# Performance work log

Measured on AMD Instinct MI355X. Metric: run time of the kernel, lower is better.

The kernel has to match this reference:

```python
import jax, jax.numpy as jnp
import numpy as np

B, T, IN_DIM = 128, 4096, 13
UNITS, MOTOR = 64, 6
LAYERS = [35, 23, 6]   # AutoNCP(64, 6): inter / command / motor neurons
_SPLITS = [35, 58]     # cumulative layer boundaries inside the 64-unit state


def setup_inputs() -> dict:
    keys = iter(jax.random.split(jax.random.key(0), 64))
    def rn(shape, s=0.1):
        return jax.random.normal(next(keys), shape, dtype=jnp.float32) * s
    inp = {"x": jax.random.normal(next(keys), (B, T, IN_DIM), dtype=jnp.float32)}
    # mixed-memory LSTM cell (ncps: input_map has bias, recurrent_map does not)
    inp["lstm_wi"] = rn((4 * UNITS, IN_DIM))
    inp["lstm_wh"] = rn((4 * UNITS, UNITS))
    inp["lstm_b"] = rn((4 * UNITS,))
    # wired CfC layers: ff1/ff2/time_a/time_b acting on concat([input, h])
    in_dims = [IN_DIM] + LAYERS[:-1]
    for i, (d, h) in enumerate(zip(in_dims, LAYERS)):
        for nm in ("w1", "w2", "wa", "wb"):
            inp[f"cfc{i}_{nm}"] = rn((h, d + h))
        for nm in ("b1", "b2", "ba", "bb"):
            inp[f"cfc{i}_{nm}"] = rn((h,))
    inp["gyro_w1"] = rn((32, MOTOR)); inp["gyro_b1"] = rn((32,))
    inp["gyro_w2"] = rn((3, 32));     inp["gyro_b2"] = rn((3,))
    inp["acc_w1"] = rn((32, MOTOR));  inp["acc_b1"] = rn((32,))
    inp["acc_w2"] = rn((3, 32));      inp["acc_b2"] = rn((3,))
    inp["unc_w1"] = rn((16, MOTOR));  inp["unc_b1"] = rn((16,))
    inp["unc_w2"] = rn((6, 16));      inp["unc_b2"] = rn((6,))
    return inp


def _cfc_step(inp, h, p):
    """ncps CfCCell, mode='default', no backbone, ts = 1.0."""
    W1, b1, W2, b2, Wa, ba, Wb, bb = p
    z = jnp.concatenate([inp, h], axis=-1)            # (B, in+hid)
    ff1 = jnp.tanh(z @ W1.T + b1)
    ff2 = jnp.tanh(z @ W2.T + b2)
    t = jax.nn.sigmoid((z @ Wa.T + ba) + (z @ Wb.T + bb))  # t_a*ts + t_b, ts==1
    return ff1 * (1.0 - t) + t * ff2


def reference(x, lstm_wi, lstm_wh, lstm_b,
              cfc0_w1, cfc0_b1, cfc0_w2, cfc0_b2, cfc0_wa, cfc0_ba, cfc0_wb, cfc0_bb,
              cfc1_w1, cfc1_b1, cfc1_w2, cfc1_b2, cfc1_wa, cfc1_ba, cfc1_wb, cfc1_bb,
              cfc2_w1, cfc2_b1, cfc2_w2, cfc2_b2, cfc2_wa, cfc2_ba, cfc2_wb, cfc2_bb,
              gyro_w1, gyro_b1, gyro_w2, gyro_b2,
              acc_w1, acc_b1, acc_w2, acc_b2,
              unc_w1, unc_b1, unc_w2, unc_b2):
    layer_params = (
        (cfc0_w1, cfc0_b1, cfc0_w2, cfc0_b2, cfc0_wa, cfc0_ba, cfc0_wb, cfc0_bb),
        (cfc1_w1, cfc1_b1, cfc1_w2, cfc1_b2, cfc1_wa, cfc1_ba, cfc1_wb, cfc1_bb),
        (cfc2_w1, cfc2_b1, cfc2_w2, cfc2_b2, cfc2_wa, cfc2_ba, cfc2_wb, cfc2_bb),
    )

    def step(carry, xt):  # xt: (B, 13)
        h, c = carry
        # mixed-memory LSTM over the full 64-unit state (forget gate +1.0)
        zg = xt @ lstm_wi.T + lstm_b + h @ lstm_wh.T
        ia, ig, fg, og = jnp.split(zg, 4, axis=-1)
        c_new = c * jax.nn.sigmoid(fg + 1.0) + jnp.tanh(ia) * jax.nn.sigmoid(ig)
        h_lstm = jnp.tanh(c_new) * jax.nn.sigmoid(og)
        # wired CfC: inter -> command -> motor, each fed previous layer's output
        hs = jnp.split(h_lstm, _SPLITS, axis=-1)
        inp = xt
        new_hs = []
        for hi, p in zip(hs, layer_params):
            inp = _cfc_step(inp, hi, p)
            new_hs.append(inp)
        return (jnp.concatenate(new_hs, axis=-1), c_new), inp  # motor out (B,6)

    Bsz = x.shape[0]
    h0 = jnp.zeros((Bsz, UNITS), x.dtype)
    c0 = jnp.zeros((Bsz, UNITS), x.dtype)
    _, outs = jax.lax.scan(step, (h0, c0), jnp.swapaxes(x, 0, 1))
    cfc_out = jnp.swapaxes(outs, 0, 1)  # (B, T, 6)

    gyro = jnp.tanh(cfc_out @ gyro_w1.T + gyro_b1) @ gyro_w2.T + gyro_b2
    acc = jnp.tanh(cfc_out @ acc_w1.T + acc_b1) @ acc_w2.T + acc_b2
    pred = jnp.concatenate([gyro, acc], axis=-1)                      # (B, T, 6)
    unc = jax.nn.softplus(
        jax.nn.relu(cfc_out @ unc_w1.T + unc_b1) @ unc_w2.T + unc_b2)  # (B, T, 6)
    return pred, unc
```

## Files before the change

kernel.cpp:

```cpp
#include <hip/hip_runtime.h>
#include <math.h>

#define BATCH 128
#define TSTEPS 4096
#define INDIM 13
#define XT 64


__device__ __forceinline__ float fsig(float x) {
    return __builtin_amdgcn_rcpf(1.f + __expf(-x));
}
__device__ __forceinline__ float ftanh(float x) {
    float s = fsig(x + x);
    return s + s - 1.f;
}
__device__ __forceinline__ float fsoftplus(float x) {
    return (x > 15.f) ? x : __logf(1.f + __expf(x));
}

__device__ __forceinline__ float qxor1(float v) {
    return __int_as_float(__builtin_amdgcn_update_dpp(
        0, __float_as_int(v), 0xB1, 0xF, 0xF, true));
}
__device__ __forceinline__ float qxor2(float v) {
    return __int_as_float(__builtin_amdgcn_update_dpp(
        0, __float_as_int(v), 0x4E, 0xF, 0xF, true));
}
#define BFLY4(a) { a += qxor1(a); a += qxor2(a); }

#define FMA4(acc, W, q, zv) { acc += zv.x * W##_##q##_0; acc += zv.y * W##_##q##_1; \
                              acc += zv.z * W##_##q##_2; acc += zv.w * W##_##q##_3; }

__global__ __launch_bounds__(256, 1)
void rnn_kernel(const float* __restrict__ x,
                const float* __restrict__ lstm_wi, const float* __restrict__ lstm_wh,
                const float* __restrict__ lstm_b,
                const float* __restrict__ c0w1, const float* __restrict__ c0w2,
                const float* __restrict__ c0wa, const float* __restrict__ c0wb,
                const float* __restrict__ c0b1, const float* __restrict__ c0b2,
                const float* __restrict__ c0ba, const float* __restrict__ c0bb,
                const float* __restrict__ c1w1, const float* __restrict__ c1w2,
                const float* __restrict__ c1wa, const float* __restrict__ c1wb,
                const float* __restrict__ c1b1, const float* __restrict__ c1b2,
                const float* __restrict__ c1ba, const float* __restrict__ c1bb,
                const float* __restrict__ c2w1, const float* __restrict__ c2w2,
                const float* __restrict__ c2wa, const float* __restrict__ c2wb,
                const float* __restrict__ c2b1, const float* __restrict__ c2b2,
                const float* __restrict__ c2ba, const float* __restrict__ c2bb,
                float* __restrict__ out)
{
    const int bb = blockIdx.x;
    const int t  = threadIdx.x;
    const int k  = t & 3;
    const int u  = t >> 2;

    __shared__ __align__(16) float smem[2688];
    float* zL  = smem;
    float* z0  = smem + 96;
    float* z1  = smem + 160;
    float* z2  = smem + 224;
    float* xt0 = smem + 256;
    float* xt1 = smem + 1088;
    float* ot0 = smem + 1920;
    float* ot1 = smem + 2304;

    const long xbase = (long)bb * TSTEPS * INDIM;
    const long obase = (long)bb * TSTEPS * 6;

    auto lwf = [&](int A, int c) -> float {
        int r = A * 64 + u;
        return (c < 13) ? lstm_wi[r * 13 + c]
             : (c < 77) ? lstm_wh[r * 64 + (c - 13)] : 0.f;
    };
#define DEF_WL(A,q) \
    float wl##A##_##q##_0 = lwf(A, 24*k + 4*q + 0); \
    float wl##A##_##q##_1 = lwf(A, 24*k + 4*q + 1); \
    float wl##A##_##q##_2 = lwf(A, 24*k + 4*q + 2); \
    float wl##A##_##q##_3 = lwf(A, 24*k + 4*q + 3);
    DEF_WL(0,0) DEF_WL(0,1) DEF_WL(0,2) DEF_WL(0,3) DEF_WL(0,4) DEF_WL(0,5)
    DEF_WL(1,0) DEF_WL(1,1) DEF_WL(1,2) DEF_WL(1,3) DEF_WL(1,4) DEF_WL(1,5)
    DEF_WL(2,0) DEF_WL(2,1) DEF_WL(2,2) DEF_WL(2,3) DEF_WL(2,4) DEF_WL(2,5)
    DEF_WL(3,0) DEF_WL(3,1) DEF_WL(3,2) DEF_WL(3,3) DEF_WL(3,4) DEF_WL(3,5)
#undef DEF_WL
    const float bL0 = lstm_b[u];
    const float bL1 = lstm_b[64 + u];
    const float bL2 = lstm_b[128 + u];
    const float bL3 = lstm_b[192 + u];

    const int grp  = (u < 35) ? 0 : (u < 58) ? 1 : 2;
    const int row  = (grp == 0) ? u : (grp == 1) ? (u - 35) : (u - 58);
    const int rl   = (grp == 0) ? 48 : (grp == 1) ? 58 : 29;
    const int clen = (grp == 0) ? 12 : (grp == 1) ? 16 : 8;
    const int cb   = clen * k;
    const float *W0p, *W1p, *W2p, *W3p;
    float bC0, bC1, bC2, bC3;
    if (grp == 0) {
        W0p = c0w1 + row * 48; W1p = c0w2 + row * 48;
        W2p = c0wa + row * 48; W3p = c0wb + row * 48;
        bC0 = c0b1[row]; bC1 = c0b2[row]; bC2 = c0ba[row]; bC3 = c0bb[row];
    } else if (grp == 1) {
        W0p = c1w1 + row * 58; W1p = c1w2 + row * 58;
        W2p = c1wa + row * 58; W3p = c1wb + row * 58;
        bC0 = c1b1[row]; bC1 = c1b2[row]; bC2 = c1ba[row]; bC3 = c1bb[row];
    } else {
        W0p = c2w1 + row * 29; W1p = c2w2 + row * 29;
        W2p = c2wa + row * 29; W3p = c2wb + row * 29;
        bC0 = c2b1[row]; bC1 = c2b2[row]; bC2 = c2ba[row]; bC3 = c2bb[row];
    }
    auto cwf = [&](const float* W, int c) -> float {
        int cc = cb + c;
        return (c < clen && cc < rl) ? W[cc] : 0.f;
    };
#define DEF_WC(A,q) \
    float wc##A##_##q##_0 = cwf(W##A##p, 4*q + 0); \
    float wc##A##_##q##_1 = cwf(W##A##p, 4*q + 1); \
    float wc##A##_##q##_2 = cwf(W##A##p, 4*q + 2); \
    float wc##A##_##q##_3 = cwf(W##A##p, 4*q + 3);
    DEF_WC(0,0) DEF_WC(0,1) DEF_WC(0,2) DEF_WC(0,3)
    DEF_WC(1,0) DEF_WC(1,1) DEF_WC(1,2) DEF_WC(1,3)
    DEF_WC(2,0) DEF_WC(2,1) DEF_WC(2,2) DEF_WC(2,3)
    DEF_WC(3,0) DEF_WC(3,1) DEF_WC(3,2) DEF_WC(3,3)
#undef DEF_WC

    float creg = 0.f;

    smem[t] = 0.f;
    if (t < 208) {
        float4 xi = *(const float4*)(x + xbase + 4 * t);
        *(float4*)&xt0[4 * t] = xi;
    }
    if (t < 13) { float x0 = x[xbase + t]; zL[t] = x0; z0[t] = x0; }
    __syncthreads();

    #pragma unroll 1
    for (int ts = 0; ts < TSTEPS; ++ts) {
        const int par = (ts >> 6) & 1;
        const int lts = ts & 63;

        {
            const float4* zc = (const float4*)(zL + 24 * k);
            float4 q0 = zc[0], q1 = zc[1], q2 = zc[2],
                   q3 = zc[3], q4 = zc[4], q5 = zc[5];
            float a0 = 0.f, a1 = 0.f, a2 = 0.f, a3 = 0.f;
            FMA4(a0, wl0, 0, q0) FMA4(a0, wl0, 1, q1) FMA4(a0, wl0, 2, q2)
            FMA4(a0, wl0, 3, q3) FMA4(a0, wl0, 4, q4) FMA4(a0, wl0, 5, q5)
            FMA4(a1, wl1, 0, q0) FMA4(a1, wl1, 1, q1) FMA4(a1, wl1, 2, q2)
            FMA4(a1, wl1, 3, q3) FMA4(a1, wl1, 4, q4) FMA4(a1, wl1, 5, q5)
            FMA4(a2, wl2, 0, q0) FMA4(a2, wl2, 1, q1) FMA4(a2, wl2, 2, q2)
            FMA4(a2, wl2, 3, q3) FMA4(a2, wl2, 4, q4) FMA4(a2, wl2, 5, q5)
            FMA4(a3, wl3, 0, q0) FMA4(a3, wl3, 1, q1) FMA4(a3, wl3, 2, q2)
            FMA4(a3, wl3, 3, q3) FMA4(a3, wl3, 4, q4) FMA4(a3, wl3, 5, q5)
            BFLY4(a0) BFLY4(a1) BFLY4(a2) BFLY4(a3)
            a0 += bL0; a1 += bL1; a2 += bL2; a3 += bL3;
            float cn = creg * fsig(a2 + 1.f) + ftanh(a0) * fsig(a1);
            creg = cn;
            float hl = ftanh(cn) * fsig(a3);
            if (k == 0) {
                if (u < 35)      z0[13 + u] = hl;
                else if (u < 58) z1[u]      = hl;
                else             z2[u - 35] = hl;
            }
        }
        __syncthreads();

        if (grp == 0) {
            const float4* zc = (const float4*)(z0 + 12 * k);
            float4 v0 = zc[0], v1 = zc[1], v2 = zc[2];
            float a0 = 0.f, a1 = 0.f, a2 = 0.f, a3 = 0.f;
            FMA4(a0, wc0, 0, v0) FMA4(a0, wc0, 1, v1) FMA4(a0, wc0, 2, v2)
            FMA4(a1, wc1, 0, v0) FMA4(a1, wc1, 1, v1) FMA4(a1, wc1, 2, v2)
            FMA4(a2, wc2, 0, v0) FMA4(a2, wc2, 1, v1) FMA4(a2, wc2, 2, v2)
            FMA4(a3, wc3, 0, v0) FMA4(a3, wc3, 1, v1) FMA4(a3, wc3, 2, v2)
            BFLY4(a0) BFLY4(a1) BFLY4(a2) BFLY4(a3)
            a0 += bC0; a1 += bC1; a2 += bC2; a3 += bC3;
            float tg = fsig(a2 + a3);
            float f1 = ftanh(a0), f2 = ftanh(a1);
            float o = f1 + tg * (f2 - f1);
            if (k == 0) { z1[row] = o; zL[13 + row] = o; }
        } else {
            if (lts == 62 && (ts + 2) < TSTEPS) {
                int i = (t - 140) * 2;
                float* dst = par ? xt0 : xt1;
                const float* src = x + xbase + (long)(ts + 2) * 13;
                if (i < 208)     *(float4*)&dst[4*i]     = *(const float4*)(src + 4*i);
                if (i + 1 < 208) *(float4*)&dst[4*(i+1)] = *(const float4*)(src + 4*(i+1));
            }
            if (lts == 0 && ts > 0) {
                int i = t - 140;
                if (i < 96) {
                    const float* src = par ? ot0 : ot1;
                    float4 v = *(const float4*)&src[4 * i];
                    *(float4*)(out + obase + (long)(ts - XT) * 6 + 4 * i) = v;
                }
            }
        }
        __syncthreads();

        if (grp == 1) {
            const float4* zc = (const float4*)(z1 + 16 * k);
            float4 v0 = zc[0], v1 = zc[1], v2 = zc[2], v3 = zc[3];
            float a0 = 0.f, a1 = 0.f, a2 = 0.f, a3 = 0.f;
            FMA4(a0, wc0, 0, v0) FMA4(a0, wc0, 1, v1) FMA4(a0, wc0, 2, v2) FMA4(a0, wc0, 3, v3)
            FMA4(a1, wc1, 0, v0) FMA4(a1, wc1, 1, v1) FMA4(a1, wc1, 2, v2) FMA4(a1, wc1, 3, v3)
            FMA4(a2, wc2, 0, v0) FMA4(a2, wc2, 1, v1) FMA4(a2, wc2, 2, v2) FMA4(a2, wc2, 3, v3)
            FMA4(a3, wc3, 0, v0) FMA4(a3, wc3, 1, v1) FMA4(a3, wc3, 2, v2) FMA4(a3, wc3, 3, v3)
            BFLY4(a0) BFLY4(a1) BFLY4(a2) BFLY4(a3)
            a0 += bC0; a1 += bC1; a2 += bC2; a3 += bC3;
            float tg = fsig(a2 + a3);
            float f1 = ftanh(a0), f2 = ftanh(a1);
            float o = f1 + tg * (f2 - f1);
            if (k == 0) { z2[row] = o; zL[48 + row] = o; }
        }
        __syncthreads();

        if (grp == 2) {
            const float4* zc = (const float4*)(z2 + 8 * k);
            float4 v0 = zc[0], v1 = zc[1];
            float a0 = 0.f, a1 = 0.f, a2 = 0.f, a3 = 0.f;
            FMA4(a0, wc0, 0, v0) FMA4(a0, wc0, 1, v1)
            FMA4(a1, wc1, 0, v0) FMA4(a1, wc1, 1, v1)
            FMA4(a2, wc2, 0, v0) FMA4(a2, wc2, 1, v1)
            FMA4(a3, wc3, 0, v0) FMA4(a3, wc3, 1, v1)
            BFLY4(a0) BFLY4(a1) BFLY4(a2) BFLY4(a3)
            a0 += bC0; a1 += bC1; a2 += bC2; a3 += bC3;
            float tg = fsig(a2 + a3);
            float f1 = ftanh(a0), f2 = ftanh(a1);
            float o = f1 + tg * (f2 - f1);
            if (k == 0) {
                zL[71 + row] = o;
                float* ob = par ? ot1 : ot0;
                ob[lts * 6 + row] = o;
            }
        } else if (t < 13 && (ts + 1) < TSTEPS) {
            const float* xb = (((ts + 1) >> 6) & 1) ? xt1 : xt0;
            float xn = xb[((ts + 1) & 63) * 13 + t];
            zL[t] = xn; z0[t] = xn;
        }
        __syncthreads();
    }

    if (t < 96) {
        float4 v = *(const float4*)&ot1[4 * t];
        *(float4*)(out + obase + (long)(TSTEPS - XT) * 6 + 4 * t) = v;
    }
}

#define S_GW1 0
#define S_GB1 192
#define S_GW2 224
#define S_GB2 320
#define S_AW1 323
#define S_AB1 515
#define S_AW2 547
#define S_AB2 643
#define S_UW1 646
#define S_UB1 742
#define S_UW2 758
#define S_UB2 854
#define S_TOT 860

__global__ __launch_bounds__(256)
void head_kernel(const float* __restrict__ gw1, const float* __restrict__ gb1,
                 const float* __restrict__ gw2, const float* __restrict__ gb2,
                 const float* __restrict__ aw1, const float* __restrict__ ab1,
                 const float* __restrict__ aw2, const float* __restrict__ ab2,
                 const float* __restrict__ uw1, const float* __restrict__ ub1,
                 const float* __restrict__ uw2, const float* __restrict__ ub2,
                 float* __restrict__ out)
{
    __shared__ float s[S_TOT];
    const int t = threadIdx.x;
    if (t < 192) { s[S_GW1 + t] = gw1[t]; s[S_AW1 + t] = aw1[t]; }
    if (t < 96)  { s[S_GW2 + t] = gw2[t]; s[S_AW2 + t] = aw2[t];
                   s[S_UW1 + t] = uw1[t]; s[S_UW2 + t] = uw2[t]; }
    if (t < 32)  { s[S_GB1 + t] = gb1[t]; s[S_AB1 + t] = ab1[t]; }
    if (t < 16)  { s[S_UB1 + t] = ub1[t]; }
    if (t < 3)   { s[S_GB2 + t] = gb2[t]; s[S_AB2 + t] = ab2[t]; }
    if (t < 6)   { s[S_UB2 + t] = ub2[t]; }
    __syncthreads();

    const long p = (long)blockIdx.x * 256 + t;
    const long base = p * 6;
    float m0 = out[base+0], m1 = out[base+1], m2 = out[base+2];
    float m3 = out[base+3], m4 = out[base+4], m5 = out[base+5];

    float gy0 = s[S_GB2+0], gy1 = s[S_GB2+1], gy2 = s[S_GB2+2];
    float ac0 = s[S_AB2+0], ac1 = s[S_AB2+1], ac2 = s[S_AB2+2];
    #pragma unroll
    for (int i = 0; i < 32; ++i) {
        float hg = s[S_GB1+i] + s[S_GW1+i*6+0]*m0 + s[S_GW1+i*6+1]*m1
                 + s[S_GW1+i*6+2]*m2 + s[S_GW1+i*6+3]*m3
                 + s[S_GW1+i*6+4]*m4 + s[S_GW1+i*6+5]*m5;
        hg = ftanh(hg);
        gy0 += s[S_GW2+i]*hg; gy1 += s[S_GW2+32+i]*hg; gy2 += s[S_GW2+64+i]*hg;
        float ha = s[S_AB1+i] + s[S_AW1+i*6+0]*m0 + s[S_AW1+i*6+1]*m1
                 + s[S_AW1+i*6+2]*m2 + s[S_AW1+i*6+3]*m3
                 + s[S_AW1+i*6+4]*m4 + s[S_AW1+i*6+5]*m5;
        ha = ftanh(ha);
        ac0 += s[S_AW2+i]*ha; ac1 += s[S_AW2+32+i]*ha; ac2 += s[S_AW2+64+i]*ha;
    }
    float u0 = s[S_UB2+0], u1 = s[S_UB2+1], u2 = s[S_UB2+2];
    float u3 = s[S_UB2+3], u4 = s[S_UB2+4], u5 = s[S_UB2+5];
    #pragma unroll
    for (int i = 0; i < 16; ++i) {
        float hu = s[S_UB1+i] + s[S_UW1+i*6+0]*m0 + s[S_UW1+i*6+1]*m1
                 + s[S_UW1+i*6+2]*m2 + s[S_UW1+i*6+3]*m3
                 + s[S_UW1+i*6+4]*m4 + s[S_UW1+i*6+5]*m5;
        hu = fmaxf(hu, 0.f);
        u0 += s[S_UW2+i]*hu;      u1 += s[S_UW2+16+i]*hu; u2 += s[S_UW2+32+i]*hu;
        u3 += s[S_UW2+48+i]*hu;   u4 += s[S_UW2+64+i]*hu; u5 += s[S_UW2+80+i]*hu;
    }
    out[base+0] = gy0; out[base+1] = gy1; out[base+2] = gy2;
    out[base+3] = ac0; out[base+4] = ac1; out[base+5] = ac2;
    const long uoff = (long)BATCH * TSTEPS * 6;
    out[uoff+base+0] = fsoftplus(u0); out[uoff+base+1] = fsoftplus(u1);
    out[uoff+base+2] = fsoftplus(u2); out[uoff+base+3] = fsoftplus(u3);
    out[uoff+base+4] = fsoftplus(u4); out[uoff+base+5] = fsoftplus(u5);
}

extern "C" void kernel_launch(void* const* d_in, const int* in_sizes, int n_in,
                              void* d_out, int out_size, void* d_ws, size_t ws_size,
                              hipStream_t stream) {
    const float* x       = (const float*)d_in[0];
    const float* lstm_wi = (const float*)d_in[1];
    const float* lstm_wh = (const float*)d_in[2];
    const float* lstm_b  = (const float*)d_in[3];
    const float* c0w1 = (const float*)d_in[4];
    const float* c0w2 = (const float*)d_in[5];
    const float* c0wa = (const float*)d_in[6];
    const float* c0wb = (const float*)d_in[7];
    const float* c0b1 = (const float*)d_in[8];
    const float* c0b2 = (const float*)d_in[9];
    const float* c0ba = (const float*)d_in[10];
    const float* c0bb = (const float*)d_in[11];
    const float* c1w1 = (const float*)d_in[12];
    const float* c1w2 = (const float*)d_in[13];
    const float* c1wa = (const float*)d_in[14];
    const float* c1wb = (const float*)d_in[15];
    const float* c1b1 = (const float*)d_in[16];
    const float* c1b2 = (const float*)d_in[17];
    const float* c1ba = (const float*)d_in[18];
    const float* c1bb = (const float*)d_in[19];
    const float* c2w1 = (const float*)d_in[20];
    const float* c2w2 = (const float*)d_in[21];
    const float* c2wa = (const float*)d_in[22];
    const float* c2wb = (const float*)d_in[23];
    const float* c2b1 = (const float*)d_in[24];
    const float* c2b2 = (const float*)d_in[25];
    const float* c2ba = (const float*)d_in[26];
    const float* c2bb = (const float*)d_in[27];
    const float* gw1 = (const float*)d_in[28];
    const float* gb1 = (const float*)d_in[29];
    const float* gw2 = (const float*)d_in[30];
    const float* gb2 = (const float*)d_in[31];
    const float* aw1 = (const float*)d_in[32];
    const float* ab1 = (const float*)d_in[33];
    const float* aw2 = (const float*)d_in[34];
    const float* ab2 = (const float*)d_in[35];
    const float* uw1 = (const float*)d_in[36];
    const float* ub1 = (const float*)d_in[37];
    const float* uw2 = (const float*)d_in[38];
    const float* ub2 = (const float*)d_in[39];
    float* out = (float*)d_out;

    rnn_kernel<<<BATCH, 256, 0, stream>>>(x, lstm_wi, lstm_wh, lstm_b,
        c0w1, c0w2, c0wa, c0wb, c0b1, c0b2, c0ba, c0bb,
        c1w1, c1w2, c1wa, c1wb, c1b1, c1b2, c1ba, c1bb,
        c2w1, c2w2, c2wa, c2wb, c2b1, c2b2, c2ba, c2bb, out);

    head_kernel<<<(BATCH * TSTEPS) / 256, 256, 0, stream>>>(
        gw1, gb1, gw2, gb2, aw1, ab1, aw2, ab2, uw1, ub1, uw2, ub2, out);
}
```

Before: 5.327 ms.

## Process two batch sequences per block to share barriers and add ILP

Each block now runs the recurrence for two batch elements, interleaving their LSTM and CfC step computations, with shared-memory state, input tiles and output staging duplicated per sequence. The grid is halved to 64 blocks. The aim is to spread the fixed per-step barrier and latency cost over two independent dependency chains, giving the scheduler more independent work to overlap. The trade-off is roughly twice the arithmetic per step on the critical path and half as many blocks, which may lengthen each step if the latency is not fully hidden.

```diff
diff --git a/kernel.cpp b/kernel.cpp
--- a/kernel.cpp
+++ b/kernel.cpp
@@ -49,23 +49,16 @@
                 const float* __restrict__ c2ba, const float* __restrict__ c2bb,
                 float* __restrict__ out)
 {
-    const int bb = blockIdx.x;
     const int t  = threadIdx.x;
     const int k  = t & 3;
     const int u  = t >> 2;
 
-    __shared__ __align__(16) float smem[2688];
-    float* zL  = smem;
-    float* z0  = smem + 96;
-    float* z1  = smem + 160;
-    float* z2  = smem + 224;
-    float* xt0 = smem + 256;
-    float* xt1 = smem + 1088;
-    float* ot0 = smem + 1920;
-    float* ot1 = smem + 2304;
-
-    const long xbase = (long)bb * TSTEPS * INDIM;
-    const long obase = (long)bb * TSTEPS * 6;
+    __shared__ __align__(16) float smem[5376];
+
+    const long xbase[2] = {(long)(2*blockIdx.x)     * TSTEPS * INDIM,
+                           (long)(2*blockIdx.x + 1) * TSTEPS * INDIM};
+    const long obase[2] = {(long)(2*blockIdx.x)     * TSTEPS * 6,
+                           (long)(2*blockIdx.x + 1) * TSTEPS * 6};
 
     auto lwf = [&](int A, int c) -> float {
         int r = A * 64 + u;
@@ -122,14 +115,16 @@
     DEF_WC(3,0) DEF_WC(3,1) DEF_WC(3,2) DEF_WC(3,3)
 #undef DEF_WC
 
-    float creg = 0.f;
-
-    smem[t] = 0.f;
+    float creg[2] = {0.f, 0.f};
+
+    for (int i = t; i < 512; i += 256) smem[i] = 0.f;
     if (t < 208) {
-        float4 xi = *(const float4*)(x + xbase + 4 * t);
-        *(float4*)&xt0[4 * t] = xi;
-    }
-    if (t < 13) { float x0 = x[xbase + t]; zL[t] = x0; z0[t] = x0; }
+        *(float4*)&smem[512 + 4*t]        = *(const float4*)(x + xbase[0] + 4*t);
+        *(float4*)&smem[512 + 1664 + 4*t] = *(const float4*)(x + xbase[1] + 4*t);
+    }
+    if (t < 13)               { float v = x[xbase[0] + t]; smem[t] = v; smem[96 + t] = v; }
+    if (t >= 16 && t < 29)    { int i = t - 16;
+                                float v = x[xbase[1] + i]; smem[256 + i] = v; smem[256 + 96 + i] = v; }
     __syncthreads();
 
     #pragma unroll 1
@@ -138,110 +133,143 @@
         const int lts = ts & 63;
 
         {
-            const float4* zc = (const float4*)(zL + 24 * k);
-            float4 q0 = zc[0], q1 = zc[1], q2 = zc[2],
-                   q3 = zc[3], q4 = zc[4], q5 = zc[5];
-            float a0 = 0.f, a1 = 0.f, a2 = 0.f, a3 = 0.f;
-            FMA4(a0, wl0, 0, q0) FMA4(a0, wl0, 1, q1) FMA4(a0, wl0, 2, q2)
-            FMA4(a0, wl0, 3, q3) FMA4(a0, wl0, 4, q4) FMA4(a0, wl0, 5, q5)
-            FMA4(a1, wl1, 0, q0) FMA4(a1, wl1, 1, q1) FMA4(a1, wl1, 2, q2)
-            FMA4(a1, wl1, 3, q3) FMA4(a1, wl1, 4, q4) FMA4(a1, wl1, 5, q5)
-            FMA4(a2, wl2, 0, q0) FMA4(a2, wl2, 1, q1) FMA4(a2, wl2, 2, q2)
-            FMA4(a2, wl2, 3, q3) FMA4(a2, wl2, 4, q4) FMA4(a2, wl2, 5, q5)
-            FMA4(a3, wl3, 0, q0) FMA4(a3, wl3, 1, q1) FMA4(a3, wl3, 2, q2)
-            FMA4(a3, wl3, 3, q3) FMA4(a3, wl3, 4, q4) FMA4(a3, wl3, 5, q5)
-            BFLY4(a0) BFLY4(a1) BFLY4(a2) BFLY4(a3)
-            a0 += bL0; a1 += bL1; a2 += bL2; a3 += bL3;
-            float cn = creg * fsig(a2 + 1.f) + ftanh(a0) * fsig(a1);
-            creg = cn;
-            float hl = ftanh(cn) * fsig(a3);
-            if (k == 0) {
-                if (u < 35)      z0[13 + u] = hl;
-                else if (u < 58) z1[u]      = hl;
-                else             z2[u - 35] = hl;
+            float4 q[2][6];
+            #pragma unroll
+            for (int e = 0; e < 2; ++e) {
+                const float4* zc = (const float4*)(smem + e*256 + 24*k);
+                q[e][0]=zc[0]; q[e][1]=zc[1]; q[e][2]=zc[2];
+                q[e][3]=zc[3]; q[e][4]=zc[4]; q[e][5]=zc[5];
+            }
+            #pragma unroll
+            for (int e = 0; e < 2; ++e) {
+                float a0 = 0.f, a1 = 0.f, a2 = 0.f, a3 = 0.f;
+                FMA4(a0, wl0, 0, q[e][0]) FMA4(a0, wl0, 1, q[e][1]) FMA4(a0, wl0, 2, q[e][2])
+                FMA4(a0, wl0, 3, q[e][3]) FMA4(a0, wl0, 4, q[e][4]) FMA4(a0, wl0, 5, q[e][5])
+                FMA4(a1, wl1, 0, q[e][0]) FMA4(a1, wl1, 1, q[e][1]) FMA4(a1, wl1, 2, q[e][2])
+                FMA4(a1, wl1, 3, q[e][3]) FMA4(a1, wl1, 4, q[e][4]) FMA4(a1, wl1, 5, q[e][5])
+                FMA4(a2, wl2, 0, q[e][0]) FMA4(a2, wl2, 1, q[e][1]) FMA4(a2, wl2, 2, q[e][2])
+                FMA4(a2, wl2, 3, q[e][3]) FMA4(a2, wl2, 4, q[e][4]) FMA4(a2, wl2, 5, q[e][5])
+                FMA4(a3, wl3, 0, q[e][0]) FMA4(a3, wl3, 1, q[e][1]) FMA4(a3, wl3, 2, q[e][2])
+                FMA4(a3, wl3, 3, q[e][3]) FMA4(a3, wl3, 4, q[e][4]) FMA4(a3, wl3, 5, q[e][5])
+                BFLY4(a0) BFLY4(a1) BFLY4(a2) BFLY4(a3)
+                a0 += bL0; a1 += bL1; a2 += bL2; a3 += bL3;
+                float cn = creg[e] * fsig(a2 + 1.f) + ftanh(a0) * fsig(a1);
+                creg[e] = cn;
+                float hl = ftanh(cn) * fsig(a3);
+                if (k == 0) {
+                    if (u < 35)      smem[e*256 + 96 + 13 + u] = hl;
+                    else if (u < 58) smem[e*256 + 160 + u]     = hl;
+                    else             smem[e*256 + 224 + (u-35)] = hl;
+                }
             }
         }
         __syncthreads();
 
         if (grp == 0) {
-            const float4* zc = (const float4*)(z0 + 12 * k);
-            float4 v0 = zc[0], v1 = zc[1], v2 = zc[2];
-            float a0 = 0.f, a1 = 0.f, a2 = 0.f, a3 = 0.f;
-            FMA4(a0, wc0, 0, v0) FMA4(a0, wc0, 1, v1) FMA4(a0, wc0, 2, v2)
-            FMA4(a1, wc1, 0, v0) FMA4(a1, wc1, 1, v1) FMA4(a1, wc1, 2, v2)
-            FMA4(a2, wc2, 0, v0) FMA4(a2, wc2, 1, v1) FMA4(a2, wc2, 2, v2)
-            FMA4(a3, wc3, 0, v0) FMA4(a3, wc3, 1, v1) FMA4(a3, wc3, 2, v2)
-            BFLY4(a0) BFLY4(a1) BFLY4(a2) BFLY4(a3)
-            a0 += bC0; a1 += bC1; a2 += bC2; a3 += bC3;
-            float tg = fsig(a2 + a3);
-            float f1 = ftanh(a0), f2 = ftanh(a1);
-            float o = f1 + tg * (f2 - f1);
-            if (k == 0) { z1[row] = o; zL[13 + row] = o; }
+            #pragma unroll
+            for (int e = 0; e < 2; ++e) {
+                const float4* zc = (const float4*)(smem + e*256 + 96 + 12*k);
+                float4 v0 = zc[0], v1 = zc[1], v2 = zc[2];
+                float a0 = 0.f, a1 = 0.f, a2 = 0.f, a3 = 0.f;
+                FMA4(a0, wc0, 0, v0) FMA4(a0, wc0, 1, v1) FMA4(a0, wc0, 2, v2)
+                FMA4(a1, wc1, 0, v0) FMA4(a1, wc1, 1, v1) FMA4(a1, wc1, 2, v2)
+                FMA4(a2, wc2, 0, v0) FMA4(a2, wc2, 1, v1) FMA4(a2, wc2, 2, v2)
+                FMA4(a3, wc3, 0, v0) FMA4(a3, wc3, 1, v1) FMA4(a3, wc3, 2, v2)
+                BFLY4(a0) BFLY4(a1) BFLY4(a2) BFLY4(a3)
+                a0 += bC0; a1 += bC1; a2 += bC2; a3 += bC3;
+                float tg = fsig(a2 + a3);
+                float f1 = ftanh(a0), f2 = ftanh(a1);
+                float o = f1 + tg * (f2 - f1);
+                if (k == 0) { smem[e*256 + 160 + row] = o;
+                              smem[e*256 + 13 + row]  = o; }
+            }
         } else {
             if (lts == 62 && (ts + 2) < TSTEPS) {
                 int i = (t - 140) * 2;
-                float* dst = par ? xt0 : xt1;
-                const float* src = x + xbase + (long)(ts + 2) * 13;
-                if (i < 208)     *(float4*)&dst[4*i]     = *(const float4*)(src + 4*i);
-                if (i + 1 < 208) *(float4*)&dst[4*(i+1)] = *(const float4*)(src + 4*(i+1));
+                #pragma unroll
+                for (int e = 0; e < 2; ++e) {
+                    float* dst = smem + 512 + e*1664 + (par ^ 1)*832;
+                    const float* src = x + xbase[e] + (long)(ts + 2) * 13;
+                    if (i < 208)     *(float4*)&dst[4*i]     = *(const float4*)(src + 4*i);
+                    if (i + 1 < 208) *(float4*)&dst[4*(i+1)] = *(const float4*)(src + 4*(i+1));
+                }
             }
             if (lts == 0 && ts > 0) {
                 int i = t - 140;
                 if (i < 96) {
-                    const float* src = par ? ot0 : ot1;
-                    float4 v = *(const float4*)&src[4 * i];
-                    *(float4*)(out + obase + (long)(ts - XT) * 6 + 4 * i) = v;
+                    #pragma unroll
+                    for (int e = 0; e < 2; ++e) {
+                        const float* src = smem + 3840 + e*768 + (par ^ 1)*384;
+                        float4 v = *(const float4*)&src[4 * i];
+                        *(float4*)(out + obase[e] + (long)(ts - XT) * 6 + 4 * i) = v;
+                    }
                 }
             }
         }
         __syncthreads();
 
         if (grp == 1) {
-            const float4* zc = (const float4*)(z1 + 16 * k);
-            float4 v0 = zc[0], v1 = zc[1], v2 = zc[2], v3 = zc[3];
-            float a0 = 0.f, a1 = 0.f, a2 = 0.f, a3 = 0.f;
-            FMA4(a0, wc0, 0, v0) FMA4(a0, wc0, 1, v1) FMA4(a0, wc0, 2, v2) FMA4(a0, wc0, 3, v3)
-            FMA4(a1, wc1, 0, v0) FMA4(a1, wc1, 1, v1) FMA4(a1, wc1, 2, v2) FMA4(a1, wc1, 3, v3)
-            FMA4(a2, wc2, 0, v0) FMA4(a2, wc2, 1, v1) FMA4(a2, wc2, 2, v2) FMA4(a2, wc2, 3, v3)
-            FMA4(a3, wc3, 0, v0) FMA4(a3, wc3, 1, v1) FMA4(a3, wc3, 2, v2) FMA4(a3, wc3, 3, v3)
-            BFLY4(a0) BFLY4(a1) BFLY4(a2) BFLY4(a3)
-            a0 += bC0; a1 += bC1; a2 += bC2; a3 += bC3;
-            float tg = fsig(a2 + a3);
-            float f1 = ftanh(a0), f2 = ftanh(a1);
-            float o = f1 + tg * (f2 - f1);
-            if (k == 0) { z2[row] = o; zL[48 + row] = o; }
+            #pragma unroll
+            for (int e = 0; e < 2; ++e) {
+                const float4* zc = (const float4*)(smem + e*256 + 160 + 16*k);
+                float4 v0 = zc[0], v1 = zc[1], v2 = zc[2], v3 = zc[3];
+                float a0 = 0.f, a1 = 0.f, a2 = 0.f, a3 = 0.f;
+                FMA4(a0, wc0, 0, v0) FMA4(a0, wc0, 1, v1) FMA4(a0, wc0, 2, v2) FMA4(a0, wc0, 3, v3)
+                FMA4(a1, wc1, 0, v0) FMA4(a1, wc1, 1, v1) FMA4(a1, wc1, 2, v2) FMA4(a1, wc1, 3, v3)
+                FMA4(a2, wc2, 0, v0) FMA4(a2, wc2, 1, v1) FMA4(a2, wc2, 2, v2) FMA4(a2, wc2, 3, v3)
+                FMA4(a3, wc3, 0, v0) FMA4(a3, wc3, 1, v1) FMA4(a3, wc3, 2, v2) FMA4(a3, wc3, 3, v3)
+                BFLY4(a0) BFLY4(a1) BFLY4(a2) BFLY4(a3)
+                a0 += bC0; a1 += bC1; a2 += bC2; a3 += bC3;
+                float tg = fsig(a2 + a3);
+                float f1 = ftanh(a0), f2 = ftanh(a1);
+                float o = f1 + tg * (f2 - f1);
+                if (k == 0) { smem[e*256 + 224 + row] = o;
+                              smem[e*256 + 48 + row]  = o; }
+            }
         }
         __syncthreads();
 
         if (grp == 2) {
-            const float4* zc = (const float4*)(z2 + 8 * k);
-            float4 v0 = zc[0], v1 = zc[1];
-            float a0 = 0.f, a1 = 0.f, a2 = 0.f, a3 = 0.f;
-            FMA4(a0, wc0, 0, v0) FMA4(a0, wc0, 1, v1)
-            FMA4(a1, wc1, 0, v0) FMA4(a1, wc1, 1, v1)
-            FMA4(a2, wc2, 0, v0) FMA4(a2, wc2, 1, v1)
-            FMA4(a3, wc3, 0, v0) FMA4(a3, wc3, 1, v1)
-            BFLY4(a0) BFLY4(a1) BFLY4(a2) BFLY4(a3)
-            a0 += bC0; a1 += bC1; a2 += bC2; a3 += bC3;
-            float tg = fsig(a2 + a3);
-            float f1 = ftanh(a0), f2 = ftanh(a1);
-            float o = f1 + tg * (f2 - f1);
-            if (k == 0) {
-                zL[71 + row] = o;
-                float* ob = par ? ot1 : ot0;
-                ob[lts * 6 + row] = o;
+            #pragma unroll
+            for (int e = 0; e < 2; ++e) {
+                const float4* zc = (const float4*)(smem + e*256 + 224 + 8*k);
+                float4 v0 = zc[0], v1 = zc[1];
+                float a0 = 0.f, a1 = 0.f, a2 = 0.f, a3 = 0.f;
+                FMA4(a0, wc0, 0, v0) FMA4(a0, wc0, 1, v1)
+                FMA4(a1, wc1, 0, v0) FMA4(a1, wc1, 1, v1)
+                FMA4(a2, wc2, 0, v0) FMA4(a2, wc2, 1, v1)
+                FMA4(a3, wc3, 0, v0) FMA4(a3, wc3, 1, v1)
+                BFLY4(a0) BFLY4(a1) BFLY4(a2) BFLY4(a3)
+                a0 += bC0; a1 += bC1; a2 += bC2; a3 += bC3;
+                float tg = fsig(a2 + a3);
+                float f1 = ftanh(a0), f2 = ftanh(a1);
+                float o = f1 + tg * (f2 - f1);
+                if (k == 0) {
+                    smem[e*256 + 71 + row] = o;
+                    float* ob = smem + 3840 + e*768 + par*384;
+                    ob[lts * 6 + row] = o;
+                }
             }
         } else if (t < 13 && (ts + 1) < TSTEPS) {
-            const float* xb = (((ts + 1) >> 6) & 1) ? xt1 : xt0;
+            const float* xb = smem + 512 + (((ts + 1) >> 6) & 1)*832;
             float xn = xb[((ts + 1) & 63) * 13 + t];
-            zL[t] = xn; z0[t] = xn;
+            smem[t] = xn; smem[96 + t] = xn;
+        } else if (t >= 16 && t < 29 && (ts + 1) < TSTEPS) {
+            const int i = t - 16;
+            const float* xb = smem + 512 + 1664 + (((ts + 1) >> 6) & 1)*832;
+            float xn = xb[((ts + 1) & 63) * 13 + i];
+            smem[256 + i] = xn; smem[256 + 96 + i] = xn;
         }
         __syncthreads();
     }
 
     if (t < 96) {
-        float4 v = *(const float4*)&ot1[4 * t];
-        *(float4*)(out + obase + (long)(TSTEPS - XT) * 6 + 4 * t) = v;
+        #pragma unroll
+        for (int e = 0; e < 2; ++e) {
+            const float* otb = smem + 3840 + e*768 + 384;
+            float4 v = *(const float4*)&otb[4 * t];
+            *(float4*)(out + obase[e] + (long)(TSTEPS - XT) * 6 + 4 * t) = v;
+        }
     }
 }
 
@@ -363,7 +391,7 @@
     const float* ub2 = (const float*)d_in[39];
     float* out = (float*)d_out;
 
-    rnn_kernel<<<BATCH, 256, 0, stream>>>(x, lstm_wi, lstm_wh, lstm_b,
+    rnn_kernel<<<BATCH / 2, 256, 0, stream>>>(x, lstm_wi, lstm_wh, lstm_b,
         c0w1, c0w2, c0wa, c0wb, c0b1, c0b2, c0ba, c0bb,
         c1w1, c1w2, c1wa, c1wb, c1b1, c1b2, c1ba, c1bb,
         c2w1, c2w2, c2wa, c2wb, c2b1, c2b2, c2ba, c2bb, out);
```

Measured after the change: 9.494 ms. 78.2% more time.

## Pack two batch sequences per 512-thread block in the recurrent kernel

Applied to the files above, without the earlier changes.

Each block now runs two independent batch rows, using two 256-thread halves with separate shared-memory regions, and the grid is halved. The intent is to improve latency hiding by interleaving two recurrences on one CU. The costs are that block-wide barriers now couple both sequences, fewer CUs are occupied, and the new launch bounds may constrain register allocation for the register-resident weights.

```diff
diff --git a/kernel.cpp b/kernel.cpp
--- a/kernel.cpp
+++ b/kernel.cpp
@@ -31,7 +31,7 @@
 #define FMA4(acc, W, q, zv) { acc += zv.x * W##_##q##_0; acc += zv.y * W##_##q##_1; \
                               acc += zv.z * W##_##q##_2; acc += zv.w * W##_##q##_3; }
 
-__global__ __launch_bounds__(256, 1)
+__global__ __launch_bounds__(512, 2)
 void rnn_kernel(const float* __restrict__ x,
                 const float* __restrict__ lstm_wi, const float* __restrict__ lstm_wh,
                 const float* __restrict__ lstm_b,
@@ -49,23 +49,25 @@
                 const float* __restrict__ c2ba, const float* __restrict__ c2bb,
                 float* __restrict__ out)
 {
-    const int bb = blockIdx.x;
-    const int t  = threadIdx.x;
-    const int k  = t & 3;
-    const int u  = t >> 2;
-
-    __shared__ __align__(16) float smem[2688];
-    float* zL  = smem;
-    float* z0  = smem + 96;
-    float* z1  = smem + 160;
-    float* z2  = smem + 224;
-    float* xt0 = smem + 256;
-    float* xt1 = smem + 1088;
-    float* ot0 = smem + 1920;
-    float* ot1 = smem + 2304;
-
-    const long xbase = (long)bb * TSTEPS * INDIM;
-    const long obase = (long)bb * TSTEPS * 6;
+    const int tid = threadIdx.x;
+    const int e   = tid >> 8;
+    const int t   = tid & 255;
+    const int k   = t & 3;
+    const int u   = t >> 2;
+
+    __shared__ __align__(16) float smem[5376];
+    float* sm  = smem + e * 2688;
+    float* zL  = sm;
+    float* z0  = sm + 96;
+    float* z1  = sm + 160;
+    float* z2  = sm + 224;
+    float* xt0 = sm + 256;
+    float* xt1 = sm + 1088;
+    float* ot0 = sm + 1920;
+    float* ot1 = sm + 2304;
+
+    const long xbase = (long)(2 * blockIdx.x + e) * TSTEPS * INDIM;
+    const long obase = (long)(2 * blockIdx.x + e) * TSTEPS * 6;
 
     auto lwf = [&](int A, int c) -> float {
         int r = A * 64 + u;
@@ -124,7 +126,7 @@
 
     float creg = 0.f;
 
-    smem[t] = 0.f;
+    sm[t] = 0.f;
     if (t < 208) {
         float4 xi = *(const float4*)(x + xbase + 4 * t);
         *(float4*)&xt0[4 * t] = xi;
@@ -363,7 +365,7 @@
     const float* ub2 = (const float*)d_in[39];
     float* out = (float*)d_out;
 
-    rnn_kernel<<<BATCH, 256, 0, stream>>>(x, lstm_wi, lstm_wh, lstm_b,
+    rnn_kernel<<<BATCH / 2, 512, 0, stream>>>(x, lstm_wi, lstm_wh, lstm_b,
         c0w1, c0w2, c0wa, c0wb, c0b1, c0b2, c0ba, c0bb,
         c1w1, c1w2, c1wa, c1wb, c1b1, c1b2, c1ba, c1bb,
         c2w1, c2w2, c2wa, c2wb, c2b1, c2b2, c2ba, c2bb, out);
```

Result: slower. 6.819 ms (+28.0%).

## Fuse command and motor CfC layers into one wavefront to drop a barrier

Applied to the files above, without the earlier changes.

Moves the command (23 units) and motor (6 units) CfC layers onto the last wavefront (threads 192-255), with 2 lanes per neuron and 32-wide register weight slices. Both layers now run in sequence inside that single wave, separated only by an LDS waitcnt fence, which removes one block-wide __syncthreads per timestep. The cost is more per-lane FMA work (32 columns instead of 16 or 8), a larger register footprint for 128 weight floats, and a fence-only ordering between the command write and the motor read within the wave.

```diff
diff --git a/kernel.cpp b/kernel.cpp
--- a/kernel.cpp
+++ b/kernel.cpp
@@ -30,6 +30,9 @@
 
 #define FMA4(acc, W, q, zv) { acc += zv.x * W##_##q##_0; acc += zv.y * W##_##q##_1; \
                               acc += zv.z * W##_##q##_2; acc += zv.w * W##_##q##_3; }
+
+#define LDS_FENCE() { asm volatile("s_waitcnt lgkmcnt(0)" ::: "memory"); \
+                      __builtin_amdgcn_sched_barrier(0); }
 
 __global__ __launch_bounds__(256, 1)
 void rnn_kernel(const float* __restrict__ x,
@@ -87,40 +90,58 @@
     const float bL2 = lstm_b[128 + u];
     const float bL3 = lstm_b[192 + u];
 
-    const int grp  = (u < 35) ? 0 : (u < 58) ? 1 : 2;
-    const int row  = (grp == 0) ? u : (grp == 1) ? (u - 35) : (u - 58);
-    const int rl   = (grp == 0) ? 48 : (grp == 1) ? 58 : 29;
-    const int clen = (grp == 0) ? 12 : (grp == 1) ? 16 : 8;
-    const int cb   = clen * k;
-    const float *W0p, *W1p, *W2p, *W3p;
-    float bC0, bC1, bC2, bC3;
-    if (grp == 0) {
-        W0p = c0w1 + row * 48; W1p = c0w2 + row * 48;
-        W2p = c0wa + row * 48; W3p = c0wb + row * 48;
-        bC0 = c0b1[row]; bC1 = c0b2[row]; bC2 = c0ba[row]; bC3 = c0bb[row];
-    } else if (grp == 1) {
-        W0p = c1w1 + row * 58; W1p = c1w2 + row * 58;
-        W2p = c1wa + row * 58; W3p = c1wb + row * 58;
-        bC0 = c1b1[row]; bC1 = c1b2[row]; bC2 = c1ba[row]; bC3 = c1bb[row];
-    } else {
-        W0p = c2w1 + row * 29; W1p = c2w2 + row * 29;
-        W2p = c2wa + row * 29; W3p = c2wb + row * 29;
-        bC0 = c2b1[row]; bC1 = c2b2[row]; bC2 = c2ba[row]; bC3 = c2bb[row];
-    }
-    auto cwf = [&](const float* W, int c) -> float {
-        int cc = cb + c;
-        return (c < clen && cc < rl) ? W[cc] : 0.f;
+    const bool g0 = (t < 140);
+    auto c0f = [&](const float* W, int j) -> float {
+        return g0 ? W[u * 48 + 12 * k + j] : 0.f;
     };
 #define DEF_WC(A,q) \
-    float wc##A##_##q##_0 = cwf(W##A##p, 4*q + 0); \
-    float wc##A##_##q##_1 = cwf(W##A##p, 4*q + 1); \
-    float wc##A##_##q##_2 = cwf(W##A##p, 4*q + 2); \
-    float wc##A##_##q##_3 = cwf(W##A##p, 4*q + 3);
-    DEF_WC(0,0) DEF_WC(0,1) DEF_WC(0,2) DEF_WC(0,3)
-    DEF_WC(1,0) DEF_WC(1,1) DEF_WC(1,2) DEF_WC(1,3)
-    DEF_WC(2,0) DEF_WC(2,1) DEF_WC(2,2) DEF_WC(2,3)
-    DEF_WC(3,0) DEF_WC(3,1) DEF_WC(3,2) DEF_WC(3,3)
+    float wc##A##_##q##_0 = c0f(C##A, 4*q + 0); \
+    float wc##A##_##q##_1 = c0f(C##A, 4*q + 1); \
+    float wc##A##_##q##_2 = c0f(C##A, 4*q + 2); \
+    float wc##A##_##q##_3 = c0f(C##A, 4*q + 3);
+    const float *C0 = c0w1, *C1 = c0w2, *C2 = c0wa, *C3 = c0wb;
+    DEF_WC(0,0) DEF_WC(0,1) DEF_WC(0,2)
+    DEF_WC(1,0) DEF_WC(1,1) DEF_WC(1,2)
+    DEF_WC(2,0) DEF_WC(2,1) DEF_WC(2,2)
+    DEF_WC(3,0) DEF_WC(3,1) DEF_WC(3,2)
 #undef DEF_WC
+    const float bC0 = g0 ? c0b1[u] : 0.f;
+    const float bC1 = g0 ? c0b2[u] : 0.f;
+    const float bC2 = g0 ? c0ba[u] : 0.f;
+    const float bC3 = g0 ? c0bb[u] : 0.f;
+
+    const int  l3   = t - 192;
+    const bool isC1 = (t >= 192) && (l3 < 46);
+    const bool isC2 = (t >= 192) && (l3 >= 46) && (l3 < 58);
+    const int  c1u  = (l3 >= 0) ? (l3 >> 1) : 0;
+    const int  c1h  = (l3 >= 0) ? (l3 & 1) : 0;
+    const int  c2u  = isC2 ? ((l3 - 46) >> 1) : 0;
+    const int  c2h  = isC2 ? ((l3 - 46) & 1) : 0;
+    float wd0[32], wd1[32], wd2[32], wd3[32];
+    {
+        const float* W1s[4] = {c1w1, c1w2, c1wa, c1wb};
+        const float* W2s[4] = {c2w1, c2w2, c2wa, c2wb};
+        float* wds[4] = {wd0, wd1, wd2, wd3};
+        #pragma unroll
+        for (int g = 0; g < 4; ++g) {
+            #pragma unroll
+            for (int j = 0; j < 32; ++j) {
+                float v = 0.f;
+                if (isC1) {
+                    const int col = 32 * c1h + j;
+                    if (col < 58) v = W1s[g][c1u * 58 + col];
+                } else if (isC2 && j < 16) {
+                    const int col = 16 * c2h + j;
+                    if (col < 29) v = W2s[g][c2u * 29 + col];
+                }
+                wds[g][j] = v;
+            }
+        }
+    }
+    const float bD0 = isC1 ? c1b1[c1u] : isC2 ? c2b1[c2u] : 0.f;
+    const float bD1 = isC1 ? c1b2[c1u] : isC2 ? c2b2[c2u] : 0.f;
+    const float bD2 = isC1 ? c1ba[c1u] : isC2 ? c2ba[c2u] : 0.f;
+    const float bD3 = isC1 ? c1bb[c1u] : isC2 ? c2bb[c2u] : 0.f;
 
     float creg = 0.f;
 
@@ -163,7 +184,7 @@
         }
         __syncthreads();
 
-        if (grp == 0) {
+        if (t < 140) {
             const float4* zc = (const float4*)(z0 + 12 * k);
             float4 v0 = zc[0], v1 = zc[1], v2 = zc[2];
             float a0 = 0.f, a1 = 0.f, a2 = 0.f, a3 = 0.f;
@@ -176,7 +197,7 @@
             float tg = fsig(a2 + a3);
             float f1 = ftanh(a0), f2 = ftanh(a1);
             float o = f1 + tg * (f2 - f1);
-            if (k == 0) { z1[row] = o; zL[13 + row] = o; }
+            if (k == 0) { z1[u] = o; zL[13 + u] = o; }
         } else {
             if (lts == 62 && (ts + 2) < TSTEPS) {
                 int i = (t - 140) * 2;
@@ -196,40 +217,52 @@
         }
         __syncthreads();
 
-        if (grp == 1) {
-            const float4* zc = (const float4*)(z1 + 16 * k);
-            float4 v0 = zc[0], v1 = zc[1], v2 = zc[2], v3 = zc[3];
-            float a0 = 0.f, a1 = 0.f, a2 = 0.f, a3 = 0.f;
-            FMA4(a0, wc0, 0, v0) FMA4(a0, wc0, 1, v1) FMA4(a0, wc0, 2, v2) FMA4(a0, wc0, 3, v3)
-            FMA4(a1, wc1, 0, v0) FMA4(a1, wc1, 1, v1) FMA4(a1, wc1, 2, v2) FMA4(a1, wc1, 3, v3)
-            FMA4(a2, wc2, 0, v0) FMA4(a2, wc2, 1, v1) FMA4(a2, wc2, 2, v2) FMA4(a2, wc2, 3, v3)
-            FMA4(a3, wc3, 0, v0) FMA4(a3, wc3, 1, v1) FMA4(a3, wc3, 2, v2) FMA4(a3, wc3, 3, v3)
-            BFLY4(a0) BFLY4(a1) BFLY4(a2) BFLY4(a3)
-            a0 += bC0; a1 += bC1; a2 += bC2; a3 += bC3;
-            float tg = fsig(a2 + a3);
-            float f1 = ftanh(a0), f2 = ftanh(a1);
-            float o = f1 + tg * (f2 - f1);
-            if (k == 0) { z2[row] = o; zL[48 + row] = o; }
-        }
-        __syncthreads();
-
-        if (grp == 2) {
-            const float4* zc = (const float4*)(z2 + 8 * k);
-            float4 v0 = zc[0], v1 = zc[1];
-            float a0 = 0.f, a1 = 0.f, a2 = 0.f, a3 = 0.f;
-            FMA4(a0, wc0, 0, v0) FMA4(a0, wc0, 1, v1)
-            FMA4(a1, wc1, 0, v0) FMA4(a1, wc1, 1, v1)
-            FMA4(a2, wc2, 0, v0) FMA4(a2, wc2, 1, v1)
-            FMA4(a3, wc3, 0, v0) FMA4(a3, wc3, 1, v1)
-            BFLY4(a0) BFLY4(a1) BFLY4(a2) BFLY4(a3)
-            a0 += bC0; a1 += bC1; a2 += bC2; a3 += bC3;
-            float tg = fsig(a2 + a3);
-            float f1 = ftanh(a0), f2 = ftanh(a1);
-            float o = f1 + tg * (f2 - f1);
-            if (k == 0) {
-                zL[71 + row] = o;
-                float* ob = par ? ot1 : ot0;
-                ob[lts * 6 + row] = o;
+        if (t >= 192) {
+            {
+                const float4* zc = (const float4*)(z1 + 32 * c1h);
+                float4 v0 = zc[0], v1 = zc[1], v2 = zc[2], v3 = zc[3],
+                       v4 = zc[4], v5 = zc[5], v6 = zc[6], v7 = zc[7];
+                const float opv[32] = {v0.x,v0.y,v0.z,v0.w, v1.x,v1.y,v1.z,v1.w,
+                                       v2.x,v2.y,v2.z,v2.w, v3.x,v3.y,v3.z,v3.w,
+                                       v4.x,v4.y,v4.z,v4.w, v5.x,v5.y,v5.z,v5.w,
+                                       v6.x,v6.y,v6.z,v6.w, v7.x,v7.y,v7.z,v7.w};
+                float a0 = 0.f, a1 = 0.f, a2 = 0.f, a3 = 0.f;
+                #pragma unroll
+                for (int j = 0; j < 32; ++j) {
+                    a0 += opv[j] * wd0[j]; a1 += opv[j] * wd1[j];
+                    a2 += opv[j] * wd2[j]; a3 += opv[j] * wd3[j];
+                }
+                a0 += qxor1(a0); a1 += qxor1(a1);
+                a2 += qxor1(a2); a3 += qxor1(a3);
+                a0 += bD0; a1 += bD1; a2 += bD2; a3 += bD3;
+                float tg = fsig(a2 + a3);
+                float f1 = ftanh(a0), f2 = ftanh(a1);
+                float o = f1 + tg * (f2 - f1);
+                if (isC1 && c1h == 0) { z2[c1u] = o; zL[48 + c1u] = o; }
+            }
+            LDS_FENCE();
+            {
+                const float4* zc = (const float4*)(z2 + 16 * c2h);
+                float4 v0 = zc[0], v1 = zc[1], v2 = zc[2], v3 = zc[3];
+                const float opv[16] = {v0.x,v0.y,v0.z,v0.w, v1.x,v1.y,v1.z,v1.w,
+                                       v2.x,v2.y,v2.z,v2.w, v3.x,v3.y,v3.z,v3.w};
+                float a0 = 0.f, a1 = 0.f, a2 = 0.f, a3 = 0.f;
+                #pragma unroll
+                for (int j = 0; j < 16; ++j) {
+                    a0 += opv[j] * wd0[j]; a1 += opv[j] * wd1[j];
+                    a2 += opv[j] * wd2[j]; a3 += opv[j] * wd3[j];
+                }
+                a0 += qxor1(a0); a1 += qxor1(a1);
+                a2 += qxor1(a2); a3 += qxor1(a3);
+                a0 += bD0; a1 += bD1; a2 += bD2; a3 += bD3;
+                float tg = fsig(a2 + a3);
+                float f1 = ftanh(a0), f2 = ftanh(a1);
+                float o = f1 + tg * (f2 - f1);
+                if (isC2 && c2h == 0) {
+                    zL[71 + c2u] = o;
+                    float* ob = par ? ot1 : ot0;
+                    ob[lts * 6 + c2u] = o;
+                }
             }
         } else if (t < 13 && (ts + 1) < TSTEPS) {
             const float* xb = (((ts + 1) >> 6) & 1) ? xt1 : xt0;
```

New measurement: 6.359 ms. +19.4%, slower.
